# Kernel optimization log

Hardware: AMD Instinct MI355X
Metric: run time of the kernel (lower is better)

## Reference

```python
import jax, jax.numpy as jnp
import numpy as np

# Assumed semantics of the undefined helpers (standard for this repo's Gaussian-splat encoder):
#   SemanticGaussianVocab.get_params(ids) -> per-token mu [B,S,d_s], log_var [B,S,d_s],
#       alpha [B,S] (sigmoid of a learned scalar embedding), features [B,S,d_f].
#   gaussian_kernel_diag(q, mu, log_var, tau) = exp(-0.5 * sum((q-mu)^2 / exp(log_var)) / tau)  -> [B,S]
#   render(features, alpha, K) : w = alpha*K; weights = w / (sum_s w + 1e-8); meaning = sum_s weights*features

V, DS, DF, NP_, MAXPOS = 32000, 64, 300, 4, 512
B, S = 256, 512
LN_EPS = 1e-5


def setup_inputs() -> dict:
    key = jax.random.key(0)
    ks = jax.random.split(key, 20)
    f32 = jnp.float32
    inp = {
        "token_ids": jax.random.randint(ks[0], (B, S), 0, V),
        "mask": jnp.ones((B, S), dtype=bool),
        # vocab tables
        "mu_table": jax.random.normal(ks[1], (V, DS), f32) * 0.02,
        "logvar_table": jax.random.normal(ks[2], (V, DS), f32) * 0.02,
        "alpha_table": jax.random.normal(ks[3], (V,), f32) * 0.02,
        "feat_table": jax.random.normal(ks[4], (V, DF), f32) * 0.02,
        # scalar log(tau)
        "log_tau": jnp.log(jnp.asarray(64.0, f32)),
        # positional embeddings (init per module: normal(std=0.01) / zeros)
        "pos_mu": jax.random.normal(ks[5], (MAXPOS, DS), f32) * 0.01,
        "pos_alpha": jnp.zeros((MAXPOS, 1), f32),
        # per-pass refinement params, stacked over n_passes-1 = 3
        "mu_W": jax.random.normal(ks[6], (NP_ - 1, DS, 2 * DF), f32) * 0.02,
        "mu_b": jnp.zeros((NP_ - 1, DS), f32),
        "gate_W": jax.random.normal(ks[7], (NP_ - 1, 1, 2 * DF), f32) * 0.02,
        "gate_b": jnp.zeros((NP_ - 1, 1), f32),
        "ln_g": jnp.ones((NP_ - 1, 2 * DF), f32),
        "ln_b": jnp.zeros((NP_ - 1, 2 * DF), f32),
        "ffn_W1": jax.random.normal(ks[8], (NP_ - 1, 2 * DF, 2 * DF), f32) * 0.02,
        "ffn_b1": jnp.zeros((NP_ - 1, 2 * DF), f32),
        "ffn_W2": jax.random.normal(ks[9], (NP_ - 1, DF, 2 * DF), f32) * 0.02,
        "ffn_b2": jnp.zeros((NP_ - 1, DF), f32),
    }
    return inp


def _encode(token_ids, mask, mu_table, logvar_table, alpha_table, feat_table,
            log_tau, pos_mu, pos_alpha, mu_W, mu_b, gate_W, gate_b,
            ln_g, ln_b, ffn_W1, ffn_b1, ffn_W2, ffn_b2):
    Bq, Sq = token_ids.shape
    mu = mu_table[token_ids]                   # [B,S,ds]
    log_var = logvar_table[token_ids]          # [B,S,ds]
    alpha = jax.nn.sigmoid(alpha_table[token_ids])  # [B,S]
    features = feat_table[token_ids]           # [B,S,df]

    pos = jnp.clip(jnp.arange(Sq), 0, MAXPOS - 1)
    mu = mu + pos_mu[pos][None]
    alpha = alpha * jax.nn.sigmoid(pos_alpha[pos][:, 0])[None]

    m = mask.astype(features.dtype)            # [B,S]
    alpha = alpha * m
    tau = jnp.exp(log_tau)
    inv_var = jnp.exp(-log_var)

    meaning = None
    for p in range(NP_):
        # masked centroid of means
        lengths = jnp.clip(m.sum(1, keepdims=True), 1.0)     # [B,1]
        centroid = (mu * m[..., None]).sum(1) / lengths       # [B,ds]
        # gaussian kernel with diagonal covariance, tempered by tau
        diff = centroid[:, None, :] - mu                       # [B,S,ds]
        d2 = jnp.sum(diff * diff * inv_var, axis=-1)           # [B,S]
        K = jnp.exp(-0.5 * d2 / tau) * m
        # render: alpha-weighted normalized pooling
        w = alpha * K
        weights = w / (w.sum(1, keepdims=True) + 1e-8)
        meaning = jnp.einsum('bs,bsf->bf', weights, features)  # [B,df]

        if p < NP_ - 1:
            ctx = jnp.broadcast_to(meaning[:, None, :], features.shape)
            combined = jnp.concatenate([features, ctx], axis=-1)  # [B,S,2df]
            # mu update: Linear(2df->ds) + tanh
            mu = mu + jnp.tanh(jnp.einsum('bsc,dc->bsd', combined, mu_W[p]) + mu_b[p])
            # alpha gate: Linear(2df->1) + sigmoid
            gate = jax.nn.sigmoid(
                jnp.einsum('bsc,oc->bso', combined, gate_W[p])[..., 0] + gate_b[p][0])
            alpha = alpha * gate
            # FFN: LayerNorm -> Linear(2df->2df) -> GELU(exact) -> Linear(2df->df)
            mean = combined.mean(-1, keepdims=True)
            var = combined.var(-1, keepdims=True)
            hn = (combined - mean) * jax.lax.rsqrt(var + LN_EPS) * ln_g[p] + ln_b[p]
            h1 = jax.nn.gelu(jnp.einsum('bsc,hc->bsh', hn, ffn_W1[p]) + ffn_b1[p],
                             approximate=False)
            features = features + jnp.einsum('bsh,fh->bsf', h1, ffn_W2[p]) + ffn_b2[p]
            alpha = alpha * m
    return meaning


def reference(token_ids, mask, mu_table, logvar_table, alpha_table, feat_table,
              log_tau, pos_mu, pos_alpha, mu_W, mu_b, gate_W, gate_b,
              ln_g, ln_b, ffn_W1, ffn_b1, ffn_W2, ffn_b2):
    return _encode(token_ids, mask, mu_table, logvar_table, alpha_table, feat_table,
                   log_tau, pos_mu, pos_alpha, mu_W, mu_b, gate_W, gate_b,
                   ln_g, ln_b, ffn_W1, ffn_b1, ffn_W2, ffn_b2)
```

## Files before the change

### kernel.cpp

```cpp
#include <hip/hip_runtime.h>
#include <hip/hip_bf16.h>
#include <math.h>

#define BQ 256
#define SQ 512
#define DS 64
#define DF 300
#define DC 600
#define NTOK (BQ*SQ)
#define KA 320
#define N1 640
#define N2 384
#define CH 2
#define CM (NTOK/CH)

typedef __attribute__((ext_vector_type(8))) short short8;
typedef __attribute__((ext_vector_type(4))) float floatx4;

__device__ __forceinline__ float sigmoidf_(float x){ return 1.0f/(1.0f+expf(-x)); }

__device__ __forceinline__ float erf_fast(float x){
    float ax = fabsf(x);
    float t = __builtin_amdgcn_rcpf(fmaf(0.3275911f, ax, 1.0f));
    float p = fmaf(fmaf(fmaf(fmaf(1.061405429f, t, -1.453152027f), t,
                             1.421413741f), t, -0.284496736f), t, 0.254829592f);
    p *= t;
    float e = __expf(-ax*ax);
    float r = fmaf(-p, e, 1.0f);
    return copysignf(r, x);
}
__device__ __forceinline__ float tanh_fast(float y){
    float e = __expf(2.0f*y);
    float t = __builtin_amdgcn_rcpf(e + 1.0f);
    return fmaf(-2.0f, t, 1.0f);
}

__device__ __forceinline__ unsigned short f2bf(float f){
    union { float f; unsigned u; } x; x.f = f;
    unsigned r = x.u + 0x7fffu + ((x.u >> 16) & 1u);
    return (unsigned short)(r >> 16);
}
__device__ __forceinline__ float bf2f(unsigned short h){
    union { unsigned u; float f; } x; x.u = ((unsigned)h) << 16;
    return x.f;
}

#define ASYNC16(gp, lp) \
  __builtin_amdgcn_global_load_lds((const __attribute__((address_space(1))) unsigned int*)(gp), \
                                   (__attribute__((address_space(3))) unsigned int*)(lp), 16, 0, 0)


__global__ void gather_featp(const int* __restrict__ ids, const float* __restrict__ ftab,
                             unsigned short* __restrict__ featp){
    int i = blockIdx.x*256 + threadIdx.x;
    if(i >= NTOK*80) return;
    int tok = i / 80, c4 = i - tok*80;
    int c = c4*4;
    ushort4 out;
    if(c < DF){
        float4 v = *(const float4*)(ftab + (size_t)ids[tok]*DF + c);
        out = make_ushort4(f2bf(v.x), f2bf(v.y), f2bf(v.z), f2bf(v.w));
    } else {
        out = make_ushort4(0,0,0,0);
    }
    *(ushort4*)(featp + (size_t)tok*KA + c) = out;
}

__global__ void gather_mu(const int* __restrict__ ids, const float* __restrict__ mtab,
                          const float* __restrict__ pos_mu, float* __restrict__ mu){
    int i = blockIdx.x*256 + threadIdx.x;
    if(i >= NTOK*DS) return;
    int d = i & 63, tok = i >> 6, s = tok & (SQ-1);
    mu[i] = mtab[ids[tok]*DS + d] + pos_mu[s*DS + d];
}

__global__ void gather_alpha(const int* __restrict__ ids, const float* __restrict__ atab,
                             const float* __restrict__ pos_al, float* __restrict__ alpha){
    int i = blockIdx.x*256 + threadIdx.x;
    if(i >= NTOK) return;
    int s = i & (SQ-1);
    alpha[i] = sigmoidf_(atab[ids[i]]) * sigmoidf_(pos_al[s]);
}

__global__ void wprep_w1g(const float* __restrict__ W1, const float* __restrict__ ln_g,
                          unsigned short* __restrict__ w1g){
    int i = blockIdx.x*256 + threadIdx.x;
    if(i >= 3*N1*KA) return;
    int p = i/(N1*KA), r = i%(N1*KA), n = r/KA, k = r%KA;
    float v = (n < DC && k < DF) ? ln_g[p*DC + k] * W1[((size_t)p*DC + n)*DC + k] : 0.f;
    w1g[i] = f2bf(v);
}
__global__ void wprep_w2(const float* __restrict__ W2, unsigned short* __restrict__ w2b){
    int i = blockIdx.x*256 + threadIdx.x;
    if(i >= 3*N2*N1) return;
    int p = i/(N2*N1), r = i%(N2*N1), n = r/N1, k = r%N1;
    float v = (n < DF && k < DC) ? W2[((size_t)p*DF + n)*DC + k] : 0.f;
    w2b[i] = f2bf(v);
}
__global__ void wprep_muw(const float* __restrict__ muW, unsigned short* __restrict__ muwb){
    int i = blockIdx.x*256 + threadIdx.x;
    if(i >= 3*DS*KA) return;
    int p = i/(DS*KA), r = i%(DS*KA), d = r/KA, k = r%KA;
    float v = (k < DF) ? muW[((size_t)p*DS + d)*DC + k] : 0.f;
    muwb[i] = f2bf(v);
}
__global__ void wprep_eg(const float* __restrict__ W1, const float* __restrict__ ln_g,
                         const float* __restrict__ ln_b, const float* __restrict__ b1,
                         float* __restrict__ G1, float* __restrict__ E1){
    int p = blockIdx.x / N1, n = blockIdx.x % N1;
    int lane = threadIdx.x;
    float ga = 0.f, ea = 0.f;
    if(n < DC){
        const float* wr = W1 + ((size_t)p*DC + n)*DC;
        const float* gp = ln_g + p*DC;
        const float* bp = ln_b + p*DC;
        for(int c = lane; c < DC; c += 64){ ga += gp[c]*wr[c]; ea += bp[c]*wr[c]; }
    }
    for(int off = 32; off; off >>= 1){
        ga += __shfl_down(ga, off);
        ea += __shfl_down(ea, off);
    }
    if(lane == 0){
        G1[blockIdx.x] = ga;
        E1[blockIdx.x] = (n < DC) ? (ea + b1[p*DC + n]) : 0.f;
    }
}

__global__ void centroid_kernel(const float* __restrict__ mu, float* __restrict__ cent){
    int b = blockIdx.x, tid = threadIdx.x;
    int d = tid & 63, sg = tid >> 6;
    const float* mb = mu + (size_t)b*SQ*DS;
    float acc = 0.f;
    for(int s = sg; s < SQ; s += 4) acc += mb[s*DS + d];
    __shared__ float red[256];
    red[tid] = acc; __syncthreads();
    if(tid < 64)
        cent[b*DS + tid] = (red[tid] + red[tid+64] + red[tid+128] + red[tid+192]) * (1.0f/SQ);
}

__global__ void kw_kernel(const int* __restrict__ ids, const float* __restrict__ mu,
                          const float* __restrict__ lvtab, const float* __restrict__ alpha,
                          const float* __restrict__ cent, const float* __restrict__ log_tau,
                          float* __restrict__ kw){
    int tid = threadIdx.x, wv = tid >> 6, lane = tid & 63;
    int tok = blockIdx.x*4 + wv;
    int b = tok >> 9;
    float ivv = expf(-lvtab[ids[tok]*DS + lane]);
    float diff = cent[b*DS + lane] - mu[(size_t)tok*DS + lane];
    float e = diff*diff*ivv;
    for(int off = 32; off; off >>= 1) e += __shfl_down(e, off);
    if(lane == 0){
        float tau = expf(log_tau[0]);
        kw[tok] = alpha[tok] * expf(-0.5f*e/tau);
    }
}

__global__ void meaning_part(const float* __restrict__ kw, const unsigned short* __restrict__ featp,
                             float* __restrict__ pm){
    int b = blockIdx.x, q = blockIdx.y;
    int tid = threadIdx.x;
    __shared__ float wsh[128];
    if(tid < 128) wsh[tid] = kw[b*SQ + q*128 + tid];
    __syncthreads();
    if(tid >= 160) return;
    const unsigned short* base = featp + ((size_t)(b*SQ + q*128))*KA + tid*2;
    float ax = 0.f, ay = 0.f;
    for(int s = 0; s < 128; s++){
        unsigned v = *(const unsigned*)(base + (size_t)s*KA);
        float w = wsh[s];
        ax += w * bf2f((unsigned short)(v & 0xffffu));
        ay += w * bf2f((unsigned short)(v >> 16));
    }
    float2* dst = (float2*)(pm + ((size_t)q*BQ + b)*KA + tid*2);
    *dst = make_float2(ax, ay);
}

__global__ void meaning_norm(const float* __restrict__ kw, const float* __restrict__ pm,
                             float* __restrict__ out){
    int b = blockIdx.x, tid = threadIdx.x;
    __shared__ float red[SQ];
    for(int s = tid; s < SQ; s += 320) red[s] = kw[b*SQ + s];
    __syncthreads();
    for(int str = 256; str >= 1; str >>= 1){
        if(tid < str && tid + str < SQ) red[tid] += red[tid+str];
        __syncthreads();
    }
    float inv = 1.0f / (red[0] + 1e-8f);
    if(tid < DF){
        float v = pm[(size_t)b*KA + tid] + pm[((size_t)BQ + b)*KA + tid]
                + pm[((size_t)2*BQ + b)*KA + tid] + pm[((size_t)3*BQ + b)*KA + tid];
        out[b*DF + tid] = v * inv;
    }
}

__global__ void meanctx_kernel(const float* __restrict__ kw, const float* __restrict__ pm,
                               const float* __restrict__ W1, const float* __restrict__ ln_g,
                               const float* __restrict__ muW, const float* __restrict__ gw,
                               float* __restrict__ msum, float* __restrict__ msq,
                               float* __restrict__ C4, float* __restrict__ C1,
                               float* __restrict__ C3){
    int b = blockIdx.x, tid = threadIdx.x;
    int lane = tid & 63, wv = tid >> 6;
    __shared__ float red[SQ];
    __shared__ float m_s[DF];
    __shared__ float gm_s[DF];
    __shared__ float rbuf[12];
    for(int s = tid; s < SQ; s += 256) red[s] = kw[b*SQ + s];
    __syncthreads();
    for(int str = 256; str >= 1; str >>= 1){
        if(tid < str && tid + str < SQ) red[tid] += red[tid+str];
        __syncthreads();
    }
    float inv = 1.0f / (red[0] + 1e-8f);
    for(int f = tid; f < DF; f += 256){
        float v = (pm[(size_t)b*KA + f] + pm[((size_t)BQ + b)*KA + f]
                 + pm[((size_t)2*BQ + b)*KA + f] + pm[((size_t)3*BQ + b)*KA + f]) * inv;
        m_s[f] = v;
        gm_s[f] = v * ln_g[DF + f];
    }
    __syncthreads();
    float s = 0.f, sq = 0.f, c4 = 0.f;
    for(int j = tid; j < DF; j += 256){
        float v = m_s[j];
        s += v; sq += v*v; c4 += v * gw[DF + j];
    }
    for(int off = 32; off; off >>= 1){
        s  += __shfl_down(s,  off);
        sq += __shfl_down(sq, off);
        c4 += __shfl_down(c4, off);
    }
    if(lane == 0){ rbuf[wv*3+0] = s; rbuf[wv*3+1] = sq; rbuf[wv*3+2] = c4; }
    __syncthreads();
    if(tid == 0){
        msum[b] = rbuf[0]+rbuf[3]+rbuf[6]+rbuf[9];
        msq[b]  = rbuf[1]+rbuf[4]+rbuf[7]+rbuf[10];
        C4[b]   = rbuf[2]+rbuf[5]+rbuf[8]+rbuf[11];
    }
    for(int n = tid; n < N1; n += 256){
        float acc = 0.f;
        if(n < DC){
            const float* wr = W1 + (size_t)n*DC + DF;
            for(int j = 0; j < DF; j++) acc += gm_s[j]*wr[j];
        }
        C1[b*N1 + n] = acc;
    }
    if(tid < DS){
        float acc = 0.f;
        const float* wr = muW + (size_t)tid*DC + DF;
        for(int j = 0; j < DF; j++) acc += m_s[j]*wr[j];
        C3[b*DS + tid] = acc;
    }
}

__global__ __launch_bounds__(256) void gemm1_kernel(
    const unsigned short* __restrict__ A, const unsigned short* __restrict__ Bw,
    const float* __restrict__ C1, const float* __restrict__ G1, const float* __restrict__ E1,
    const float* __restrict__ mean_t, const float* __restrict__ rstd_t,
    unsigned short* __restrict__ H1, int m_base)
{
    __shared__ __align__(16) short lA[2][128*32];
    __shared__ __align__(16) short lB[2][128*32];
    int bid = blockIdx.x;
    int n0 = (bid >> 9)*128, m0 = (bid & 511)*128;
    int g0 = m_base + m0;
    int tid = threadIdx.x, lane = tid & 63, w = tid >> 6;
    int wm = w >> 1, wn = w & 1;
    int m16 = lane & 15, quad = lane >> 4;

    floatx4 acc[4][4];
    #pragma unroll
    for(int i=0;i<4;i++)
        #pragma unroll
        for(int j=0;j<4;j++){ acc[i][j][0]=0.f; acc[i][j][1]=0.f; acc[i][j][2]=0.f; acc[i][j][3]=0.f; }

    auto issue = [&](int k0, int buf){
        #pragma unroll
        for(int i = 0; i < 2; i++){
            int c = i*256 + tid;
            ASYNC16(A + (size_t)(g0 + (c>>2))*KA + k0 + (c&3)*8, &lA[buf][c*8]);
        }
        #pragma unroll
        for(int i = 0; i < 2; i++){
            int c = i*256 + tid;
            ASYNC16(Bw + (size_t)(n0 + (c>>2))*KA + k0 + (c&3)*8, &lB[buf][c*8]);
        }
    };
    issue(0, 0);
    int cur = 0;
    #pragma unroll 1
    for(int k0 = 32; k0 <= KA; k0 += 32){
        __syncthreads();
        if(k0 < KA) issue(k0, cur^1);
        short8 af[4], bf[4];
        #pragma unroll
        for(int f = 0; f < 4; f++){
            af[f] = *(const short8*)(&lA[cur][(wm*64 + f*16 + m16)*32 + quad*8]);
            bf[f] = *(const short8*)(&lB[cur][(wn*64 + f*16 + m16)*32 + quad*8]);
        }
        #pragma unroll
        for(int fm = 0; fm < 4; fm++)
            #pragma unroll
            for(int fn = 0; fn < 4; fn++)
                acc[fm][fn] = __builtin_amdgcn_mfma_f32_16x16x32_bf16(af[fm], bf[fn], acc[fm][fn], 0,0,0);
        cur ^= 1;
    }
    int b = g0 >> 9;
    const float* C1b = C1 + b*N1;
    float c1a[4], g1a[4], e1a[4]; int cola[4];
    #pragma unroll
    for(int fn = 0; fn < 4; fn++){
        int col = n0 + wn*64 + fn*16 + m16;
        cola[fn] = col; c1a[fn] = C1b[col]; g1a[fn] = G1[col]; e1a[fn] = E1[col];
    }
    #pragma unroll
    for(int fm = 0; fm < 4; fm++){
        int rowb = m0 + wm*64 + fm*16 + quad*4;
        #pragma unroll
        for(int r = 0; r < 4; r++){
            int tl = rowb + r;
            int tg = m_base + tl;
            float rs = rstd_t[tg], mrs = -mean_t[tg]*rs;
            #pragma unroll
            for(int fn = 0; fn < 4; fn++){
                if(cola[fn] < DC){
                    float pre = rs*(acc[fm][fn][r] + c1a[fn]) + mrs*g1a[fn] + e1a[fn];
                    float gl = 0.5f*pre*(1.0f + erf_fast(pre*0.70710678118654752f));
                    H1[(size_t)tl*N1 + cola[fn]] = f2bf(gl);
                }
            }
        }
    }
}

__global__ __launch_bounds__(256) void gemm2_kernel(
    const unsigned short* __restrict__ A, const unsigned short* __restrict__ Bw,
    const float* __restrict__ b2, unsigned short* __restrict__ featp, int m_base)
{
    __shared__ __align__(16) short lA[2][128*32];
    __shared__ __align__(16) short lB[2][128*32];
    int bid = blockIdx.x;
    int n0 = (bid >> 9)*128, m0 = (bid & 511)*128;
    int tid = threadIdx.x, lane = tid & 63, w = tid >> 6;
    int wm = w >> 1, wn = w & 1;
    int m16 = lane & 15, quad = lane >> 4;

    floatx4 acc[4][4];
    #pragma unroll
    for(int i=0;i<4;i++)
        #pragma unroll
        for(int j=0;j<4;j++){ acc[i][j][0]=0.f; acc[i][j][1]=0.f; acc[i][j][2]=0.f; acc[i][j][3]=0.f; }

    auto issue = [&](int k0, int buf){
        #pragma unroll
        for(int i = 0; i < 2; i++){
            int c = i*256 + tid;
            ASYNC16(A + (size_t)(m0 + (c>>2))*N1 + k0 + (c&3)*8, &lA[buf][c*8]);
        }
        #pragma unroll
        for(int i = 0; i < 2; i++){
            int c = i*256 + tid;
            ASYNC16(Bw + (size_t)(n0 + (c>>2))*N1 + k0 + (c&3)*8, &lB[buf][c*8]);
        }
    };
    issue(0, 0);
    int cur = 0;
    #pragma unroll 1
    for(int k0 = 32; k0 <= N1; k0 += 32){
        __syncthreads();
        if(k0 < N1) issue(k0, cur^1);
        short8 af[4], bf[4];
        #pragma unroll
        for(int f = 0; f < 4; f++){
            af[f] = *(const short8*)(&lA[cur][(wm*64 + f*16 + m16)*32 + quad*8]);
            bf[f] = *(const short8*)(&lB[cur][(wn*64 + f*16 + m16)*32 + quad*8]);
        }
        #pragma unroll
        for(int fm = 0; fm < 4; fm++)
            #pragma unroll
            for(int fn = 0; fn < 4; fn++)
                acc[fm][fn] = __builtin_amdgcn_mfma_f32_16x16x32_bf16(af[fm], bf[fn], acc[fm][fn], 0,0,0);
        cur ^= 1;
    }
    #pragma unroll
    for(int fn = 0; fn < 4; fn++){
        int col = n0 + wn*64 + fn*16 + m16;
        if(col < DF){
            float bb = b2[col];
            #pragma unroll
            for(int fm = 0; fm < 4; fm++){
                int rowb = m0 + wm*64 + fm*16 + quad*4;
                #pragma unroll
                for(int r = 0; r < 4; r++){
                    size_t idx = (size_t)(m_base + rowb + r)*KA + col;
                    featp[idx] = f2bf(bf2f(featp[idx]) + acc[fm][fn][r] + bb);
                }
            }
        }
    }
}

__global__ __launch_bounds__(256) void gemm3_kernel(
    const unsigned short* __restrict__ A, const unsigned short* __restrict__ Bw,
    const float* __restrict__ C3, const float* __restrict__ mub, float* __restrict__ mu,
    const float* __restrict__ gw, const float* __restrict__ gate_b,
    const float* __restrict__ C4, const float* __restrict__ msum,
    const float* __restrict__ msq, float* __restrict__ mean_t,
    float* __restrict__ rstd_t, float* __restrict__ alpha)
{
    __shared__ __align__(16) short lA[2][128*32];
    __shared__ __align__(16) short lB[2][64*32];
    __shared__ float gws[KA];
    __shared__ float sred[256];
    int m0 = blockIdx.x*128;
    int b = m0 >> 9;
    int tid = threadIdx.x, lane = tid & 63, wm = tid >> 6;
    int m16 = lane & 15, quad = lane >> 4;
    int rr = tid & 127, hh = tid >> 7;

    for(int i = tid; i < KA; i += 256) gws[i] = gw[i];

    floatx4 acc[2][4];
    #pragma unroll
    for(int i=0;i<2;i++)
        #pragma unroll
        for(int j=0;j<4;j++){ acc[i][j][0]=0.f; acc[i][j][1]=0.f; acc[i][j][2]=0.f; acc[i][j][3]=0.f; }

    float s_sum = 0.f, s_sq = 0.f, s_gd = 0.f;

    auto issue = [&](int k0, int buf){
        #pragma unroll
        for(int i = 0; i < 2; i++){
            int c = i*256 + tid;
            ASYNC16(A + (size_t)(m0 + (c>>2))*KA + k0 + (c&3)*8, &lA[buf][c*8]);
        }
        {
            int c = tid;
            ASYNC16(Bw + (size_t)(c>>2)*KA + k0 + (c&3)*8, &lB[buf][c*8]);
        }
    };
    issue(0, 0);
    int cur = 0;
    #pragma unroll 1
    for(int k0 = 32; k0 <= KA; k0 += 32){
        __syncthreads();
        if(k0 < KA) issue(k0, cur^1);
        short8 af[2], bf[4];
        #pragma unroll
        for(int f = 0; f < 2; f++)
            af[f] = *(const short8*)(&lA[cur][((wm*2+f)*16 + m16)*32 + quad*8]);
        #pragma unroll
        for(int f = 0; f < 4; f++)
            bf[f] = *(const short8*)(&lB[cur][(f*16 + m16)*32 + quad*8]);
        #pragma unroll
        for(int fm = 0; fm < 2; fm++)
            #pragma unroll
            for(int fn = 0; fn < 4; fn++)
                acc[fm][fn] = __builtin_amdgcn_mfma_f32_16x16x32_bf16(af[fm], bf[fn], acc[fm][fn], 0,0,0);
        {
            const short* lrow = &lA[cur][rr*32 + hh*16];
            short8 v0 = *(const short8*)(lrow);
            short8 v1 = *(const short8*)(lrow + 8);
            int cb = (k0 - 32) + hh*16;
            #pragma unroll
            for(int j = 0; j < 8; j++){
                float v = bf2f((unsigned short)v0[j]);
                s_sum += v; s_sq += v*v; s_gd += v*gws[cb + j];
            }
            #pragma unroll
            for(int j = 0; j < 8; j++){
                float v = bf2f((unsigned short)v1[j]);
                s_sum += v; s_sq += v*v; s_gd += v*gws[cb + 8 + j];
            }
        }
        cur ^= 1;
    }
    __syncthreads();
    float rowsum = 0.f, rowsq = 0.f, rowgd = 0.f;
    sred[tid] = s_sum; __syncthreads();
    if(tid < 128) rowsum = sred[tid] + sred[tid+128];
    __syncthreads();
    sred[tid] = s_sq; __syncthreads();
    if(tid < 128) rowsq = sred[tid] + sred[tid+128];
    __syncthreads();
    sred[tid] = s_gd; __syncthreads();
    if(tid < 128) rowgd = sred[tid] + sred[tid+128];
    if(tid < 128){
        int t = m0 + tid;
        float S = rowsum + msum[b], Q = rowsq + msq[b];
        float mean = S * (1.0f/DC);
        float var = fmaxf(Q * (1.0f/DC) - mean*mean, 0.f);
        mean_t[t] = mean;
        rstd_t[t] = rsqrtf(var + 1e-5f);
        alpha[t] *= sigmoidf_(rowgd + C4[b] + gate_b[0]);
    }
    const float* C3b = C3 + b*DS;
    #pragma unroll
    for(int fn = 0; fn < 4; fn++){
        int col = fn*16 + m16;
        float cc = C3b[col] + mub[col];
        #pragma unroll
        for(int fm = 0; fm < 2; fm++){
            int rowb = m0 + (wm*2+fm)*16 + quad*4;
            #pragma unroll
            for(int r = 0; r < 4; r++){
                size_t t = (size_t)(rowb + r);
                mu[t*DS + col] += tanh_fast(acc[fm][fn][r] + cc);
            }
        }
    }
}

extern "C" void kernel_launch(void* const* d_in, const int* in_sizes, int n_in,
                              void* d_out, int out_size, void* d_ws, size_t ws_size,
                              hipStream_t stream)
{
    const int*   ids      = (const int*)  d_in[0];
    const float* mu_table = (const float*)d_in[2];
    const float* lv_table = (const float*)d_in[3];
    const float* a_table  = (const float*)d_in[4];
    const float* f_table  = (const float*)d_in[5];
    const float* log_tau  = (const float*)d_in[6];
    const float* pos_mu   = (const float*)d_in[7];
    const float* pos_al   = (const float*)d_in[8];
    const float* mu_W     = (const float*)d_in[9];
    const float* mu_b     = (const float*)d_in[10];
    const float* gate_W   = (const float*)d_in[11];
    const float* gate_b   = (const float*)d_in[12];
    const float* ln_g     = (const float*)d_in[13];
    const float* ln_b     = (const float*)d_in[14];
    const float* ffn_W1   = (const float*)d_in[15];
    const float* ffn_b1   = (const float*)d_in[16];
    const float* ffn_W2   = (const float*)d_in[17];
    const float* ffn_b2   = (const float*)d_in[18];

    float* ws     = (float*)d_ws;
    float* mu     = ws;
    float* alpha  = mu     + 8388608;
    float* kw     = alpha  + 131072;
    float* cent   = kw     + 131072;
    float* meanb  = cent   + 16384;
    float* mean_t = meanb  + 76800;
    float* rstd_t = mean_t + 131072;
    float* msum   = rstd_t + 131072;
    float* msq    = msum   + 256;
    float* C4     = msq    + 256;
    float* C1     = C4     + 256;
    float* C3     = C1     + 163840;
    float* E1     = C3     + 16384;
    float* G1     = E1     + 1920;
    float* pm     = G1     + 1920;
    unsigned short* featp = (unsigned short*)(pm + 327680);
    unsigned short* w1g   = featp + (size_t)NTOK*KA;
    unsigned short* w2b   = w1g  + 3*N1*KA;
    unsigned short* muwb  = w2b  + 3*N2*N1;
    unsigned short* h1buf = muwb + 3*DS*KA;

    gather_featp<<<(NTOK*80+255)/256, 256, 0, stream>>>(ids, f_table, featp);
    gather_mu   <<<(NTOK*DS+255)/256, 256, 0, stream>>>(ids, mu_table, pos_mu, mu);
    gather_alpha<<<(NTOK+255)/256,    256, 0, stream>>>(ids, a_table, pos_al, alpha);

    wprep_w1g<<<(3*N1*KA+255)/256, 256, 0, stream>>>(ffn_W1, ln_g, w1g);
    wprep_w2 <<<(3*N2*N1+255)/256, 256, 0, stream>>>(ffn_W2, w2b);
    wprep_muw<<<(3*DS*KA+255)/256, 256, 0, stream>>>(mu_W, muwb);
    wprep_eg <<<3*N1, 64, 0, stream>>>(ffn_W1, ln_g, ln_b, ffn_b1, G1, E1);

    for(int p = 0; p < 4; p++){
        centroid_kernel<<<BQ, 256, 0, stream>>>(mu, cent);
        kw_kernel<<<NTOK/4, 256, 0, stream>>>(ids, mu, lv_table, alpha, cent, log_tau, kw);
        meaning_part<<<dim3(BQ,4), 192, 0, stream>>>(kw, featp, pm);
        if(p == 3){
            meaning_norm<<<BQ, 320, 0, stream>>>(kw, pm, (float*)d_out);
        } else {
            meanctx_kernel<<<BQ, 256, 0, stream>>>(kw, pm, ffn_W1 + (size_t)p*DC*DC,
                                                   ln_g + p*DC, mu_W + (size_t)p*DS*DC,
                                                   gate_W + p*DC, msum, msq, C4, C1, C3);
            gemm3_kernel<<<NTOK/128, 256, 0, stream>>>(featp, muwb + (size_t)p*DS*KA,
                                                       C3, mu_b + p*DS, mu,
                                                       gate_W + p*DC, gate_b + p,
                                                       C4, msum, msq, mean_t, rstd_t, alpha);
            for(int c = 0; c < CH; c++){
                gemm1_kernel<<<(CM/128)*5, 256, 0, stream>>>(featp, w1g + (size_t)p*N1*KA,
                                                             C1, G1 + p*N1, E1 + p*N1,
                                                             mean_t, rstd_t, h1buf, c*CM);
                gemm2_kernel<<<(CM/128)*3, 256, 0, stream>>>(h1buf, w2b + (size_t)p*N2*N1,
                                                             ffn_b2 + p*DF, featp, c*CM);
            }
        }
    }
}
```

Measured before the change: 1.474 ms.

## Triple-buffer LDS async loads in GEMM kernels with partial vmcnt waits

Moves the three MFMA GEMM kernels from double-buffered to triple-buffered async global-to-LDS loads. Two K-tiles are prefetched ahead, and the full __syncthreads is replaced by s_waitcnt vmcnt(N) plus s_barrier, so the next tile's loads stay in flight during compute. This hides more global memory latency. In exchange, LDS use per block rises by half, which may lower occupancy, and the hand-written waitcnt counts must match the number of loads issued per tile.

Measured after the change: 1.490 ms. Within noise of the previous version (+1.1%).

```diff
diff --git a/kernel.cpp b/kernel.cpp
--- a/kernel.cpp
+++ b/kernel.cpp
@@ -48,6 +48,8 @@
 #define ASYNC16(gp, lp) \
   __builtin_amdgcn_global_load_lds((const __attribute__((address_space(1))) unsigned int*)(gp), \
                                    (__attribute__((address_space(3))) unsigned int*)(lp), 16, 0, 0)
+
+#define PIPE_SYNC(N) asm volatile("s_waitcnt vmcnt(" #N ")\n\ts_barrier" ::: "memory")
 
 
 __global__ void gather_featp(const int* __restrict__ ids, const float* __restrict__ ftab,
@@ -258,8 +260,8 @@
     const float* __restrict__ mean_t, const float* __restrict__ rstd_t,
     unsigned short* __restrict__ H1, int m_base)
 {
-    __shared__ __align__(16) short lA[2][128*32];
-    __shared__ __align__(16) short lB[2][128*32];
+    __shared__ __align__(16) short lA[3][128*32];
+    __shared__ __align__(16) short lB[3][128*32];
     int bid = blockIdx.x;
     int n0 = (bid >> 9)*128, m0 = (bid & 511)*128;
     int g0 = m_base + m0;
@@ -286,11 +288,13 @@
         }
     };
     issue(0, 0);
+    issue(32, 1);
     int cur = 0;
     #pragma unroll 1
-    for(int k0 = 32; k0 <= KA; k0 += 32){
-        __syncthreads();
-        if(k0 < KA) issue(k0, cur^1);
+    for(int k0 = 0; k0 < KA; k0 += 32){
+        if(k0 + 32 < KA) PIPE_SYNC(4);
+        else             PIPE_SYNC(0);
+        if(k0 + 64 < KA) issue(k0 + 64, cur == 0 ? 2 : cur - 1);
         short8 af[4], bf[4];
         #pragma unroll
         for(int f = 0; f < 4; f++){
@@ -302,7 +306,7 @@
             #pragma unroll
             for(int fn = 0; fn < 4; fn++)
                 acc[fm][fn] = __builtin_amdgcn_mfma_f32_16x16x32_bf16(af[fm], bf[fn], acc[fm][fn], 0,0,0);
-        cur ^= 1;
+        cur = (cur == 2) ? 0 : cur + 1;
     }
     int b = g0 >> 9;
     const float* C1b = C1 + b*N1;
@@ -336,8 +340,8 @@
     const unsigned short* __restrict__ A, const unsigned short* __restrict__ Bw,
     const float* __restrict__ b2, unsigned short* __restrict__ featp, int m_base)
 {
-    __shared__ __align__(16) short lA[2][128*32];
-    __shared__ __align__(16) short lB[2][128*32];
+    __shared__ __align__(16) short lA[3][128*32];
+    __shared__ __align__(16) short lB[3][128*32];
     int bid = blockIdx.x;
     int n0 = (bid >> 9)*128, m0 = (bid & 511)*128;
     int tid = threadIdx.x, lane = tid & 63, w = tid >> 6;
@@ -363,11 +367,13 @@
         }
     };
     issue(0, 0);
+    issue(32, 1);
     int cur = 0;
     #pragma unroll 1
-    for(int k0 = 32; k0 <= N1; k0 += 32){
-        __syncthreads();
-        if(k0 < N1) issue(k0, cur^1);
+    for(int k0 = 0; k0 < N1; k0 += 32){
+        if(k0 + 32 < N1) PIPE_SYNC(4);
+        else             PIPE_SYNC(0);
+        if(k0 + 64 < N1) issue(k0 + 64, cur == 0 ? 2 : cur - 1);
         short8 af[4], bf[4];
         #pragma unroll
         for(int f = 0; f < 4; f++){
@@ -379,7 +385,7 @@
             #pragma unroll
             for(int fn = 0; fn < 4; fn++)
                 acc[fm][fn] = __builtin_amdgcn_mfma_f32_16x16x32_bf16(af[fm], bf[fn], acc[fm][fn], 0,0,0);
-        cur ^= 1;
+        cur = (cur == 2) ? 0 : cur + 1;
     }
     #pragma unroll
     for(int fn = 0; fn < 4; fn++){
@@ -407,8 +413,8 @@
     const float* __restrict__ msq, float* __restrict__ mean_t,
     float* __restrict__ rstd_t, float* __restrict__ alpha)
 {
-    __shared__ __align__(16) short lA[2][128*32];
-    __shared__ __align__(16) short lB[2][64*32];
+    __shared__ __align__(16) short lA[3][128*32];
+    __shared__ __align__(16) short lB[3][64*32];
     __shared__ float gws[KA];
     __shared__ float sred[256];
     int m0 = blockIdx.x*128;
@@ -418,6 +424,7 @@
     int rr = tid & 127, hh = tid >> 7;
 
     for(int i = tid; i < KA; i += 256) gws[i] = gw[i];
+    __syncthreads();
 
     floatx4 acc[2][4];
     #pragma unroll
@@ -439,11 +446,13 @@
         }
     };
     issue(0, 0);
+    issue(32, 1);
     int cur = 0;
     #pragma unroll 1
-    for(int k0 = 32; k0 <= KA; k0 += 32){
-        __syncthreads();
-        if(k0 < KA) issue(k0, cur^1);
+    for(int k0 = 0; k0 < KA; k0 += 32){
+        if(k0 + 32 < KA) PIPE_SYNC(3);
+        else             PIPE_SYNC(0);
+        if(k0 + 64 < KA) issue(k0 + 64, cur == 0 ? 2 : cur - 1);
         short8 af[2], bf[4];
         #pragma unroll
         for(int f = 0; f < 2; f++)
@@ -460,7 +469,7 @@
             const short* lrow = &lA[cur][rr*32 + hh*16];
             short8 v0 = *(const short8*)(lrow);
             short8 v1 = *(const short8*)(lrow + 8);
-            int cb = (k0 - 32) + hh*16;
+            int cb = k0 + hh*16;
             #pragma unroll
             for(int j = 0; j < 8; j++){
                 float v = bf2f((unsigned short)v0[j]);
@@ -472,7 +481,7 @@
                 s_sum += v; s_sq += v*v; s_gd += v*gws[cb + 8 + j];
             }
         }
-        cur ^= 1;
+        cur = (cur == 2) ? 0 : cur + 1;
     }
     __syncthreads();
     float rowsum = 0.f, rowsq = 0.f, rowgd = 0.f;
```
